# Kernel tuning notes

Measured on AMD Instinct MI355X. Metric: run time of the kernel, lower is better.

## Reference

```python
import math
import jax, jax.numpy as jnp
import numpy as np

S = 2048   # padded sequence length (both src and tgt)
B = 8      # batch
D = 512    # d_embed
K = 64     # num_neighbors


def setup_inputs() -> dict:
    key = jax.random.key(0)
    ks = jax.random.split(key, 12)
    f32 = jnp.float32
    src_feats = jax.random.normal(ks[0], (S, B, D), f32)
    tgt_feats = jax.random.normal(ks[1], (S, B, D), f32)
    src_xyz = jax.random.normal(ks[2], (S, B, 3), f32)
    tgt_xyz = jax.random.normal(ks[3], (S, B, 3), f32)
    # lengths in [S - S//8, S] so every row has plenty of valid keys (>= K)
    src_lens = S - jax.random.randint(ks[4], (B,), 0, S // 8)
    tgt_lens = S - jax.random.randint(ks[5], (B,), 0, S // 8)
    scale = 1.0 / math.sqrt(D)
    Wq = jax.random.normal(ks[6], (D, D), f32) * scale
    bq = jnp.zeros((D,), f32)
    Wk = jax.random.normal(ks[7], (D, D), f32) * scale
    bk = jnp.zeros((D,), f32)
    Wc = jax.random.normal(ks[8], (1, D), f32) * scale
    bc = jnp.zeros((1,), f32)
    return dict(src_feats_padded=src_feats, tgt_feats_padded=tgt_feats,
                src_xyz_padded=src_xyz, tgt_xyz_padded=tgt_xyz,
                src_lens=src_lens, tgt_lens=tgt_lens,
                Wq=Wq, bq=bq, Wk=Wk, bk=bk, Wc=Wc, bc=bc)


def _simple_attention(query, key, value, key_padding_mask, Wq, bq, Wk, bk, num_neighbors):
    # query: (Q,B,D), key: (S,B,D), value: (S,B,E), key_padding_mask: (B,S) True=pad
    d = query.shape[-1]
    q = (query @ Wq.T + bq) / math.sqrt(d)          # (Q,B,D)
    k = key @ Wk.T + bk                              # (S,B,D)
    attn = jnp.einsum('qbd,sbd->bqs', q, k)          # (B,Q,S)
    attn = attn + jnp.where(key_padding_mask, -jnp.inf, 0.0)[:, None, :]
    if num_neighbors > 0:
        # Faithful to torch's `neighbor_mask[:, :, haha] = 0` (advanced indexing):
        # the UNION of top-k column indices over all (b,q) rows is unmasked for
        # every row; all other columns get -inf.
        idx = jax.lax.top_k(attn, num_neighbors)[1]              # (B,Q,K)
        col_mask = jnp.full((attn.shape[-1],), -jnp.inf, attn.dtype)
        col_mask = col_mask.at[idx.reshape(-1)].set(0.0)         # (S,)
        attn = attn + col_mask[None, None, :]
    attn = jax.nn.softmax(attn, axis=-1)
    return jnp.einsum('bqs,sbe->qbe', attn, value)   # (Q,B,E)


def _forward(src_feats, tgt_feats, src_xyz, tgt_xyz, src_lens, tgt_lens,
             Wq, bq, Wk, bk, Wc, bc):
    n_src, b = src_feats.shape[0], src_feats.shape[1]
    n_tgt = tgt_feats.shape[0]
    src_kpm = jnp.arange(n_src)[None, :] >= src_lens[:, None]   # (B,N_src)
    tgt_kpm = jnp.arange(n_tgt)[None, :] >= tgt_lens[:, None]   # (B,N_tgt)
    src_corr = _simple_attention(src_feats, tgt_feats, tgt_xyz, tgt_kpm,
                                 Wq, bq, Wk, bk, K)             # (N_src,B,3)
    tgt_corr = _simple_attention(tgt_feats, src_feats, src_xyz, src_kpm,
                                 Wq, bq, Wk, bk, K)             # (N_tgt,B,3)
    src_overlap = src_feats @ Wc.T + bc                          # (N_src,B,1)
    tgt_overlap = tgt_feats @ Wc.T + bc                          # (N_tgt,B,1)
    return src_corr, tgt_corr, src_overlap, tgt_overlap


def reference(src_feats_padded, tgt_feats_padded, src_xyz_padded, tgt_xyz_padded,
              src_lens, tgt_lens, Wq, bq, Wk, bk, Wc, bc):
    return _forward(src_feats_padded, tgt_feats_padded, src_xyz_padded,
                    tgt_xyz_padded, src_lens, tgt_lens, Wq, bq, Wk, bk, Wc, bc)
```

## Files before the change

kernel.cpp:

```cpp
#include <hip/hip_runtime.h>

typedef __attribute__((ext_vector_type(8))) short short8;
typedef __attribute__((ext_vector_type(4))) short s16x4;
typedef __attribute__((ext_vector_type(4))) float f32x4;

#define SEQ 2048
#define BAT 8
#define DIM 512
#define RSQRT_D 0.044194173824159216f

__device__ __forceinline__ unsigned short f2bf(float x) {
  union { float f; unsigned u; } v; v.f = x;
  unsigned r = (v.u + 0x7FFFu + ((v.u >> 16) & 1u)) >> 16;
  return (unsigned short)r;
}

__device__ __forceinline__ unsigned char f2fp8(float x) {
  return (unsigned char)(__builtin_amdgcn_cvt_pk_fp8_f32(x, x, 0, false) & 0xFF);
}

__device__ __forceinline__ void gload_lds16(const void* g, void* lds_base) {
  __builtin_amdgcn_global_load_lds(
      (const __attribute__((address_space(1))) unsigned int*)g,
      (__attribute__((address_space(3))) unsigned int*)lds_base,
      16, 0, 0);
}

__device__ __forceinline__ f32x4 mfma_pv(s16x4 a, s16x4 b, f32x4 c) {
  asm("v_mfma_f32_16x16x16_bf16 %0, %1, %2, %0" : "+v"(c) : "v"(a), "v"(b));
  return c;
}

__global__ __launch_bounds__(256) void k_pack(
    const float* __restrict__ src, const float* __restrict__ tgt,
    const float* __restrict__ Wc, const float* __restrict__ bc,
    const float* __restrict__ sxyz, const float* __restrict__ txyz,
    const float* __restrict__ Wq, const float* __restrict__ Wk,
    unsigned short* __restrict__ srcT, unsigned short* __restrict__ tgtT,
    float4* __restrict__ Vsrc, float4* __restrict__ Vtgt,
    unsigned short* __restrict__ Wqb, unsigned short* __restrict__ Wkb,
    float* __restrict__ out) {
  int which = blockIdx.y;
  if (blockIdx.x >= 4096) {
    int e = (blockIdx.x - 4096) * 256 + threadIdx.x;
    if (which == 0) {
      int wsel = e >> 15, j = e & 32767;
      const float* wp = (wsel ? Wk : Wq) + (size_t)j * 8;
      unsigned short* o = wsel ? Wkb : Wqb;
      float4 f0 = *(const float4*)wp, f1 = *(const float4*)(wp + 4);
      uint4 pk;
      pk.x = (unsigned)f2bf(f0.x) | ((unsigned)f2bf(f0.y) << 16);
      pk.y = (unsigned)f2bf(f0.z) | ((unsigned)f2bf(f0.w) << 16);
      pk.z = (unsigned)f2bf(f1.x) | ((unsigned)f2bf(f1.y) << 16);
      pk.w = (unsigned)f2bf(f1.z) | ((unsigned)f2bf(f1.w) << 16);
      *(uint4*)(o + (size_t)j * 8) = pk;
    } else if (e < 32768) {
      int wsel = e >> 14, id = e & 16383;
      int s = id >> 3, b = id & 7;
      const float* xyz = (wsel ? txyz : sxyz) + (size_t)id * 3;
      float4 v = make_float4(xyz[0], xyz[1], xyz[2], 0.f);
      (wsel ? Vtgt : Vsrc)[b * SEQ + s] = v;
    }
    return;
  }
  int w = threadIdx.x >> 6, lane = threadIdx.x & 63;
  int row = blockIdx.x * 4 + w;
  const float* in = (which ? tgt : src) + (size_t)row * DIM;
  unsigned short* T = which ? tgtT : srcT;
  int s = row >> 3, b = row & 7;

  const float4* in4 = (const float4*)in;
  float4 f0 = in4[lane * 2], f1 = in4[lane * 2 + 1];

  uint4 pk;
  pk.x = (unsigned)f2bf(f0.x) | ((unsigned)f2bf(f0.y) << 16);
  pk.y = (unsigned)f2bf(f0.z) | ((unsigned)f2bf(f0.w) << 16);
  pk.z = (unsigned)f2bf(f1.x) | ((unsigned)f2bf(f1.y) << 16);
  pk.w = (unsigned)f2bf(f1.z) | ((unsigned)f2bf(f1.w) << 16);
  *(uint4*)(T + ((size_t)(b * SEQ + s) * DIM + lane * 8)) = pk;

  const float4* wc4 = (const float4*)Wc;
  float4 w0 = wc4[lane * 2], w1 = wc4[lane * 2 + 1];
  float d = f0.x * w0.x + f0.y * w0.y + f0.z * w0.z + f0.w * w0.w +
            f1.x * w1.x + f1.y * w1.y + f1.z * w1.z + f1.w * w1.w;
  for (int o = 32; o; o >>= 1) d += __shfl_xor(d, o);
  if (lane == 0) {
    int base = which ? (SEQ * BAT * 6 + SEQ * BAT) : (SEQ * BAT * 6);
    out[base + row] = d + bc[0];
  }
}

__global__ __launch_bounds__(256) void k_proj(
    const unsigned short* __restrict__ srcT, const unsigned short* __restrict__ tgtT,
    const unsigned short* __restrict__ Wqb, const unsigned short* __restrict__ Wkb,
    const float* __restrict__ bq, const float* __restrict__ bk,
    unsigned char* __restrict__ Qsrc, unsigned char* __restrict__ Ktgt,
    unsigned char* __restrict__ Qtgt, unsigned char* __restrict__ Ksrc) {
  __shared__ __align__(16) char at[16384];
  __shared__ __align__(16) char bt[16384];
  int id = blockIdx.x;
  int x = id & 7, t = id >> 3;
  int m = x * 16 + (t >> 4);
  int inner = t & 15;
  int n = inner & 3, z = inner >> 2;
  bool isQ = (z == 0 || z == 2);
  const unsigned short* A = (z == 0 || z == 3) ? srcT : tgtT;
  const unsigned short* W = isQ ? Wqb : Wkb;
  const float* bias = isQ ? bq : bk;
  unsigned char* O = z == 0 ? Qsrc : z == 1 ? Ktgt : z == 2 ? Qtgt : Ksrc;

  int m0 = m * 128, n0 = n * 128;
  int tid = threadIdx.x, w = tid >> 6, lane = tid & 63;
  int ln = lane & 15, quad = lane >> 4;
  int moff = (w & 1) * 64, noff = (w >> 1) * 64;

  f32x4 acc[4][4];
  f32x4 zero = {0.f, 0.f, 0.f, 0.f};
  for (int mi = 0; mi < 4; ++mi)
    for (int ni = 0; ni < 4; ++ni) acc[mi][ni] = zero;

  for (int kb = 0; kb < DIM; kb += 64) {
    #pragma unroll
    for (int it = 0; it < 4; ++it) {
      int rbase = w * 32 + it * 8;
      int r = rbase + (lane >> 3);
      int c = (lane & 7) ^ (r & 7);
      gload_lds16(A + ((size_t)(m0 + r) * DIM + kb + c * 8), &at[rbase * 128]);
      gload_lds16(W + ((size_t)(n0 + r) * DIM + kb + c * 8), &bt[rbase * 128]);
    }
    __syncthreads();
    #pragma unroll
    for (int ks = 0; ks < 2; ++ks) {
      short8 afr[4], bfr[4];
      #pragma unroll
      for (int mi = 0; mi < 4; ++mi) {
        int r = moff + mi * 16 + ln;
        int p = (ks * 4 + quad) ^ (r & 7);
        afr[mi] = *(const short8*)(&at[r * 128 + p * 16]);
      }
      #pragma unroll
      for (int ni = 0; ni < 4; ++ni) {
        int r = noff + ni * 16 + ln;
        int p = (ks * 4 + quad) ^ (r & 7);
        bfr[ni] = *(const short8*)(&bt[r * 128 + p * 16]);
      }
      #pragma unroll
      for (int mi = 0; mi < 4; ++mi)
        #pragma unroll
        for (int ni = 0; ni < 4; ++ni)
          acc[mi][ni] = __builtin_amdgcn_mfma_f32_16x16x32_bf16(afr[mi], bfr[ni], acc[mi][ni], 0, 0, 0);
    }
    __syncthreads();
  }

  for (int ni = 0; ni < 4; ++ni) {
    int n_g = n0 + noff + ni * 16 + ln;
    float bv = bias[n_g];
    for (int mi = 0; mi < 4; ++mi) {
      int m_g = m0 + moff + mi * 16 + quad * 4;
      for (int r = 0; r < 4; ++r) {
        float v = acc[mi][ni][r] + bv;
        int row = m_g + r;
        size_t pos;
        if (isQ) pos = (size_t)row * DIM + n_g;
        else     pos = (size_t)row * DIM + ((((n_g >> 3) ^ (row & 15)) << 3) | (n_g & 7));
        O[pos] = f2fp8(v);
      }
    }
  }
}

__global__ __launch_bounds__(256) void k_attn(
    const unsigned char* __restrict__ Qsrc, const unsigned char* __restrict__ Ktgt,
    const unsigned char* __restrict__ Qtgt, const unsigned char* __restrict__ Ksrc,
    const float4* __restrict__ Vsrc, const float4* __restrict__ Vtgt,
    const int* __restrict__ src_lens, const int* __restrict__ tgt_lens,
    float4* __restrict__ part) {
  __shared__ __align__(16) char klds[16384];
  __shared__ __align__(16) char vaug[4096];
  int id = blockIdx.x;
  int x = id & 7, j = id >> 3;
  int group = (j >> 6) * 8 + x;
  int dir = group >> 3, b = group & 7;
  int inner = j & 63;
  int chunk = inner >> 4, qb = inner & 15;

  const unsigned char* Q = dir ? Qtgt : Qsrc;
  const unsigned char* K = dir ? Ksrc : Ktgt;
  const float4* V = dir ? Vsrc : Vtgt;
  int len = (dir ? src_lens : tgt_lens)[b];
  int k0g = chunk * 512;
  int kend = min(len, k0g + 512);
  int nblk = (kend - k0g + 31) >> 5;

  int tid = threadIdx.x, w = tid >> 6, lane = tid & 63;
  int ln = lane & 15, quad = lane >> 4;
  int q0 = qb * 128 + w * 16;

  if (tid < 128) {
    int rem = kend - k0g;
    const float4* vsrc = V + b * SEQ + k0g + tid * 4;
    float c[4][4];
    #pragma unroll
    for (int jj = 0; jj < 4; ++jj) {
      float4 vv = vsrc[jj];
      bool val = (tid * 4 + jj) < rem;
      c[0][jj] = val ? 1.f : 0.f;
      c[1][jj] = val ? vv.x : 0.f;
      c[2][jj] = val ? vv.y : 0.f;
      c[3][jj] = val ? vv.z : 0.f;
    }
    uint4 w0, w1;
    w0.x = (unsigned)f2bf(c[0][0]) | ((unsigned)f2bf(c[0][1]) << 16);
    w0.y = (unsigned)f2bf(c[0][2]) | ((unsigned)f2bf(c[0][3]) << 16);
    w0.z = (unsigned)f2bf(c[1][0]) | ((unsigned)f2bf(c[1][1]) << 16);
    w0.w = (unsigned)f2bf(c[1][2]) | ((unsigned)f2bf(c[1][3]) << 16);
    w1.x = (unsigned)f2bf(c[2][0]) | ((unsigned)f2bf(c[2][1]) << 16);
    w1.y = (unsigned)f2bf(c[2][2]) | ((unsigned)f2bf(c[2][3]) << 16);
    w1.z = (unsigned)f2bf(c[3][0]) | ((unsigned)f2bf(c[3][1]) << 16);
    w1.w = (unsigned)f2bf(c[3][2]) | ((unsigned)f2bf(c[3][3]) << 16);
    *(uint4*)(vaug + tid * 32) = w0;
    *(uint4*)(vaug + tid * 32 + 16) = w1;
  }

  long af[16], ag[16];
  {
    const unsigned char* qrowA = Q + (size_t)(b * SEQ + q0 + ln) * DIM + quad * 8;
    const unsigned char* qrowB = qrowA + (size_t)64 * DIM;
    #pragma unroll
    for (int kk = 0; kk < 16; ++kk) {
      af[kk] = *(const long*)(qrowA + kk * 32);
      ag[kk] = *(const long*)(qrowB + kk * 32);
    }
  }

  f32x4 accPV0 = {0.f, 0.f, 0.f, 0.f};
  f32x4 accPV1 = {0.f, 0.f, 0.f, 0.f};
  const unsigned char* kchunk = K + (size_t)(b * SEQ + k0g) * DIM;

  for (int kb = 0; kb < nblk; ++kb) {
    const unsigned char* kbase = kchunk + (size_t)kb * 32 * DIM;
    #pragma unroll
    for (int it = 0; it < 4; ++it) {
      int rp = w * 4 + it;
      gload_lds16(kbase + rp * 1024 + lane * 16, &klds[rp * 1024]);
    }
    __syncthreads();

    const char* krow0 = klds + ln * DIM;
    const char* krow1 = krow0 + 16 * DIM;

    f32x4 acc0 = {0.f, 0.f, 0.f, 0.f}, acc1 = {0.f, 0.f, 0.f, 0.f};
    f32x4 acc2 = {0.f, 0.f, 0.f, 0.f}, acc3 = {0.f, 0.f, 0.f, 0.f};
    __builtin_amdgcn_s_setprio(1);
    #pragma unroll
    for (int kk = 0; kk < 16; ++kk) {
      int pos = (((kk * 4 + quad) ^ ln) << 3);
      long b0 = *(const long*)(krow0 + pos);
      long b1 = *(const long*)(krow1 + pos);
      acc0 = __builtin_amdgcn_mfma_f32_16x16x32_fp8_fp8(b0, af[kk], acc0, 0, 0, 0);
      acc1 = __builtin_amdgcn_mfma_f32_16x16x32_fp8_fp8(b1, af[kk], acc1, 0, 0, 0);
      acc2 = __builtin_amdgcn_mfma_f32_16x16x32_fp8_fp8(b0, ag[kk], acc2, 0, 0, 0);
      acc3 = __builtin_amdgcn_mfma_f32_16x16x32_fp8_fp8(b1, ag[kk], acc3, 0, 0, 0);
    }
    __builtin_amdgcn_s_setprio(0);

    union U { unsigned u[2]; s16x4 s; };
    U pA0, pA1, pB0, pB1;
    {
      float p0 = __expf(acc0[0] * RSQRT_D), p1 = __expf(acc0[1] * RSQRT_D);
      float p2 = __expf(acc0[2] * RSQRT_D), p3 = __expf(acc0[3] * RSQRT_D);
      asm("v_cvt_pk_bf16_f32 %0, %1, %2" : "=v"(pA0.u[0]) : "v"(p0), "v"(p1));
      asm("v_cvt_pk_bf16_f32 %0, %1, %2" : "=v"(pA0.u[1]) : "v"(p2), "v"(p3));
      float r0 = __expf(acc1[0] * RSQRT_D), r1 = __expf(acc1[1] * RSQRT_D);
      float r2 = __expf(acc1[2] * RSQRT_D), r3 = __expf(acc1[3] * RSQRT_D);
      asm("v_cvt_pk_bf16_f32 %0, %1, %2" : "=v"(pA1.u[0]) : "v"(r0), "v"(r1));
      asm("v_cvt_pk_bf16_f32 %0, %1, %2" : "=v"(pA1.u[1]) : "v"(r2), "v"(r3));
      float s0 = __expf(acc2[0] * RSQRT_D), s1 = __expf(acc2[1] * RSQRT_D);
      float s2 = __expf(acc2[2] * RSQRT_D), s3 = __expf(acc2[3] * RSQRT_D);
      asm("v_cvt_pk_bf16_f32 %0, %1, %2" : "=v"(pB0.u[0]) : "v"(s0), "v"(s1));
      asm("v_cvt_pk_bf16_f32 %0, %1, %2" : "=v"(pB0.u[1]) : "v"(s2), "v"(s3));
      float t0 = __expf(acc3[0] * RSQRT_D), t1 = __expf(acc3[1] * RSQRT_D);
      float t2 = __expf(acc3[2] * RSQRT_D), t3 = __expf(acc3[3] * RSQRT_D);
      asm("v_cvt_pk_bf16_f32 %0, %1, %2" : "=v"(pB1.u[0]) : "v"(t0), "v"(t1));
      asm("v_cvt_pk_bf16_f32 %0, %1, %2" : "=v"(pB1.u[1]) : "v"(t2), "v"(t3));
    }

    int voff = kb * 256 + quad * 32 + (ln & 3) * 8;
    s16x4 va0 = *(const s16x4*)(vaug + voff);
    s16x4 va1 = *(const s16x4*)(vaug + voff + 128);
    accPV0 = mfma_pv(va0, pA0.s, accPV0);
    accPV0 = mfma_pv(va1, pA1.s, accPV0);
    accPV1 = mfma_pv(va0, pB0.s, accPV1);
    accPV1 = mfma_pv(va1, pB1.s, accPV1);

    __syncthreads();
  }

  if (quad == 0) {
    size_t base = ((size_t)(dir * BAT + b) * 4 + chunk) * SEQ;
    part[base + q0 + ln] =
        make_float4(accPV0[0], accPV0[1], accPV0[2], accPV0[3]);
    part[base + q0 + 64 + ln] =
        make_float4(accPV1[0], accPV1[1], accPV1[2], accPV1[3]);
  }
}

__global__ __launch_bounds__(256) void k_attn_reduce(
    const float4* __restrict__ part, float* __restrict__ out) {
  int t = blockIdx.x * 256 + threadIdx.x;
  int dir = t >> 14, rem = t & 16383, b = rem >> 11, q = rem & 2047;
  size_t base = ((size_t)(dir * BAT + b) * 4) * SEQ + q;
  float4 s0 = part[base];
  float4 s1 = part[base + SEQ];
  float4 s2 = part[base + 2 * SEQ];
  float4 s3 = part[base + 3 * SEQ];
  float inv = 1.f / (s0.x + s1.x + s2.x + s3.x);
  float* ob = out + (size_t)dir * (SEQ * BAT * 3) + ((size_t)q * BAT + b) * 3;
  ob[0] = (s0.y + s1.y + s2.y + s3.y) * inv;
  ob[1] = (s0.z + s1.z + s2.z + s3.z) * inv;
  ob[2] = (s0.w + s1.w + s2.w + s3.w) * inv;
}

extern "C" void kernel_launch(void* const* d_in, const int* in_sizes, int n_in,
                              void* d_out, int out_size, void* d_ws, size_t ws_size,
                              hipStream_t stream) {
  const float* src  = (const float*)d_in[0];
  const float* tgt  = (const float*)d_in[1];
  const float* sxyz = (const float*)d_in[2];
  const float* txyz = (const float*)d_in[3];
  const int* slens  = (const int*)d_in[4];
  const int* tlens  = (const int*)d_in[5];
  const float* Wq   = (const float*)d_in[6];
  const float* bq   = (const float*)d_in[7];
  const float* Wk   = (const float*)d_in[8];
  const float* bk   = (const float*)d_in[9];
  const float* Wc   = (const float*)d_in[10];
  const float* bc   = (const float*)d_in[11];
  float* out = (float*)d_out;

  char* ws = (char*)d_ws;
  size_t off = 0;
  auto carve = [&](size_t bytes) -> char* {
    char* p = ws + off;
    off += (bytes + 255) & ~(size_t)255;
    return p;
  };
  const size_t FEAT_BF  = (size_t)BAT * SEQ * DIM * 2;
  const size_t FEAT_FP8 = (size_t)BAT * SEQ * DIM;
  unsigned short* srcT = (unsigned short*)carve(FEAT_BF);
  unsigned short* tgtT = (unsigned short*)carve(FEAT_BF);
  unsigned char* Qsrc = (unsigned char*)carve(FEAT_FP8);
  unsigned char* Ktgt = (unsigned char*)carve(FEAT_FP8);
  unsigned char* Qtgt = (unsigned char*)carve(FEAT_FP8);
  unsigned char* Ksrc = (unsigned char*)carve(FEAT_FP8);
  unsigned short* Wqb  = (unsigned short*)carve((size_t)DIM * DIM * 2);
  unsigned short* Wkb  = (unsigned short*)carve((size_t)DIM * DIM * 2);
  float4* Vsrc = (float4*)carve((size_t)BAT * SEQ * 16);
  float4* Vtgt = (float4*)carve((size_t)BAT * SEQ * 16);
  float4* part = (float4*)srcT;

  k_pack<<<dim3(4352, 2), 256, 0, stream>>>(src, tgt, Wc, bc, sxyz, txyz, Wq, Wk,
                                            srcT, tgtT, Vsrc, Vtgt, Wqb, Wkb, out);
  k_proj<<<dim3(2048), 256, 0, stream>>>(srcT, tgtT, Wqb, Wkb, bq, bk,
                                         Qsrc, Ktgt, Qtgt, Ksrc);
  k_attn<<<dim3(1024), 256, 0, stream>>>(Qsrc, Ktgt, Qtgt, Ksrc, Vsrc, Vtgt,
                                         slens, tlens, part);
  k_attn_reduce<<<dim3(128), 256, 0, stream>>>(part, out);
}
```

Before: 231.3 us.

## Share activation tile between Q and K projections in one 512-thread block

New measurement: 215.8 us (median of 4 runs). 1.07x faster.

```diff
diff --git a/kernel.cpp b/kernel.cpp
--- a/kernel.cpp
+++ b/kernel.cpp
@@ -90,29 +90,29 @@
   }
 }
 
-__global__ __launch_bounds__(256) void k_proj(
+__global__ __launch_bounds__(512) void k_proj(
     const unsigned short* __restrict__ srcT, const unsigned short* __restrict__ tgtT,
     const unsigned short* __restrict__ Wqb, const unsigned short* __restrict__ Wkb,
     const float* __restrict__ bq, const float* __restrict__ bk,
     unsigned char* __restrict__ Qsrc, unsigned char* __restrict__ Ktgt,
     unsigned char* __restrict__ Qtgt, unsigned char* __restrict__ Ksrc) {
   __shared__ __align__(16) char at[16384];
-  __shared__ __align__(16) char bt[16384];
+  __shared__ __align__(16) char wqt[16384];
+  __shared__ __align__(16) char wkt[16384];
   int id = blockIdx.x;
   int x = id & 7, t = id >> 3;
-  int m = x * 16 + (t >> 4);
-  int inner = t & 15;
-  int n = inner & 3, z = inner >> 2;
-  bool isQ = (z == 0 || z == 2);
-  const unsigned short* A = (z == 0 || z == 3) ? srcT : tgtT;
-  const unsigned short* W = isQ ? Wqb : Wkb;
-  const float* bias = isQ ? bq : bk;
-  unsigned char* O = z == 0 ? Qsrc : z == 1 ? Ktgt : z == 2 ? Qtgt : Ksrc;
+  int m = x * 16 + (t >> 3);
+  int inner = t & 7;
+  int n = inner & 3, ap = inner >> 2;
+  const unsigned short* A = ap ? tgtT : srcT;
 
   int m0 = m * 128, n0 = n * 128;
   int tid = threadIdx.x, w = tid >> 6, lane = tid & 63;
   int ln = lane & 15, quad = lane >> 4;
-  int moff = (w & 1) * 64, noff = (w >> 1) * 64;
+  int grp = w >> 2, wl = w & 3;
+  int moff = (wl & 1) * 64, noff = (wl >> 1) * 64;
+  const float* bias = grp ? bk : bq;
+  unsigned char* O = grp ? (ap ? Ktgt : Ksrc) : (ap ? Qtgt : Qsrc);
 
   f32x4 acc[4][4];
   f32x4 zero = {0.f, 0.f, 0.f, 0.f};
@@ -121,14 +121,21 @@
 
   for (int kb = 0; kb < DIM; kb += 64) {
     #pragma unroll
-    for (int it = 0; it < 4; ++it) {
-      int rbase = w * 32 + it * 8;
+    for (int it = 0; it < 6; ++it) {
+      int s = w * 6 + it;
+      int tile = s >> 4, within = s & 15;
+      int rbase = within * 8;
       int r = rbase + (lane >> 3);
       int c = (lane & 7) ^ (r & 7);
-      gload_lds16(A + ((size_t)(m0 + r) * DIM + kb + c * 8), &at[rbase * 128]);
-      gload_lds16(W + ((size_t)(n0 + r) * DIM + kb + c * 8), &bt[rbase * 128]);
+      const unsigned short* g =
+          (tile == 0 ? A + (size_t)(m0 + r) * DIM
+                     : (tile == 1 ? Wqb : Wkb) + (size_t)(n0 + r) * DIM) +
+          kb + c * 8;
+      char* dst = (tile == 0 ? at : tile == 1 ? wqt : wkt) + rbase * 128;
+      gload_lds16(g, dst);
     }
     __syncthreads();
+    const char* bt = grp ? wkt : wqt;
     #pragma unroll
     for (int ks = 0; ks < 2; ++ks) {
       short8 afr[4], bfr[4];
@@ -148,24 +155,28 @@
       for (int mi = 0; mi < 4; ++mi)
         #pragma unroll
         for (int ni = 0; ni < 4; ++ni)
-          acc[mi][ni] = __builtin_amdgcn_mfma_f32_16x16x32_bf16(afr[mi], bfr[ni], acc[mi][ni], 0, 0, 0);
+          acc[mi][ni] = __builtin_amdgcn_mfma_f32_16x16x32_bf16(bfr[ni], afr[mi], acc[mi][ni], 0, 0, 0);
     }
     __syncthreads();
   }
 
+  bool isQ = (grp == 0);
+  #pragma unroll
   for (int ni = 0; ni < 4; ++ni) {
-    int n_g = n0 + noff + ni * 16 + ln;
-    float bv = bias[n_g];
+    int n_b = n0 + noff + ni * 16 + quad * 4;
+    float4 bv = *(const float4*)(bias + n_b);
+    #pragma unroll
     for (int mi = 0; mi < 4; ++mi) {
-      int m_g = m0 + moff + mi * 16 + quad * 4;
-      for (int r = 0; r < 4; ++r) {
-        float v = acc[mi][ni][r] + bv;
-        int row = m_g + r;
-        size_t pos;
-        if (isQ) pos = (size_t)row * DIM + n_g;
-        else     pos = (size_t)row * DIM + ((((n_g >> 3) ^ (row & 15)) << 3) | (n_g & 7));
-        O[pos] = f2fp8(v);
-      }
+      int row = m0 + moff + mi * 16 + ln;
+      int u;
+      u = __builtin_amdgcn_cvt_pk_fp8_f32(acc[mi][ni][0] + bv.x,
+                                          acc[mi][ni][1] + bv.y, 0, false);
+      u = __builtin_amdgcn_cvt_pk_fp8_f32(acc[mi][ni][2] + bv.z,
+                                          acc[mi][ni][3] + bv.w, u, true);
+      size_t pos;
+      if (isQ) pos = (size_t)row * DIM + n_b;
+      else     pos = (size_t)row * DIM + ((((n_b >> 3) ^ (row & 15)) << 3) | (n_b & 7));
+      *(unsigned*)(O + pos) = (unsigned)u;
     }
   }
 }
@@ -362,7 +373,7 @@
 
   k_pack<<<dim3(4352, 2), 256, 0, stream>>>(src, tgt, Wc, bc, sxyz, txyz, Wq, Wk,
                                             srcT, tgtT, Vsrc, Vtgt, Wqb, Wkb, out);
-  k_proj<<<dim3(2048), 256, 0, stream>>>(srcT, tgtT, Wqb, Wkb, bq, bk,
+  k_proj<<<dim3(1024), 512, 0, stream>>>(srcT, tgtT, Wqb, Wkb, bq, bk,
                                          Qsrc, Ktgt, Qtgt, Ksrc);
   k_attn<<<dim3(1024), 256, 0, stream>>>(Qsrc, Ktgt, Qtgt, Ksrc, Vsrc, Vtgt,
                                          slens, tlens, part);
```
